# Optimization experiments

Measured on AMD Instinct MI355X. Metric: run time of the kernel, lower is better.

Reference implementation:

```python
import jax, jax.numpy as jnp
import numpy as np

E, S, H, D, B = 8, 64, 2048, 1024, 8192
LN_EPS = 1e-5


def setup_inputs() -> dict:
    key = jax.random.key(0)
    ks = jax.random.split(key, 12)
    n = lambda k, shape: jax.random.normal(k, shape, jnp.float32) * 0.02
    return {
        "raw_state": jax.random.normal(ks[0], (B, S), jnp.float32),
        "has_proprio": jax.random.randint(ks[1], (B,), 0, 2, jnp.int32),
        "expert_idx": jax.random.randint(ks[2], (B,), 0, E, jnp.int32),
        "pw1": n(ks[3], (E, S, H)), "pb1": jnp.zeros((E, H), jnp.float32),
        "pw2": n(ks[4], (E, H, D)), "pb2": jnp.zeros((E, D), jnp.float32),
        "qw1": n(ks[5], (E, S, H)), "qb1": jnp.zeros((E, H), jnp.float32),
        "qw2": n(ks[6], (E, H, D)), "qb2": jnp.zeros((E, D), jnp.float32),
        "ln_g": jnp.ones((E, D), jnp.float32), "ln_b": jnp.zeros((E, D), jnp.float32),
        "tw1": n(ks[7], (E, D, H)), "tb1": jnp.zeros((E, H), jnp.float32),
        "tw2": n(ks[8], (E, H, D)), "tb2": jnp.zeros((E, D), jnp.float32),
    }


def _gelu(x):
    # torch nn.GELU default = exact erf form
    return jax.nn.gelu(x, approximate=False)


def _expert_fwd(x, sel, w):
    (pw1, pb1, pw2, pb2, qw1, qb1, qw2, qb2, ln_g, ln_b, tw1, tb1, tw2, tb2) = w
    placeholder = _gelu(x @ pw1 + pb1) @ pw2 + pb2      # [B, D]
    proprio = _gelu(x @ qw1 + qb1) @ qw2 + qb2          # [B, D]
    mixed = placeholder * (1.0 - sel) + proprio * sel    # [B, D]
    mu = jnp.mean(mixed, axis=-1, keepdims=True)
    var = jnp.mean(jnp.square(mixed - mu), axis=-1, keepdims=True)
    normed = (mixed - mu) * jax.lax.rsqrt(var + LN_EPS) * ln_g + ln_b
    return _gelu(normed @ tw1 + tb1) @ tw2 + tb2         # [B, D]


def reference(raw_state, has_proprio, expert_idx,
              pw1, pb1, pw2, pb2, qw1, qb1, qw2, qb2,
              ln_g, ln_b, tw1, tb1, tw2, tb2):
    sel = has_proprio.astype(raw_state.dtype)[:, None]  # [B, 1]
    n_experts = pw1.shape[0]
    acc = jnp.zeros((raw_state.shape[0], tw2.shape[-1]), raw_state.dtype)
    # Fixed small loop over experts; rows routed via mask-select (same math
    # as the original index_select -> projector -> index_copy_).
    for e in range(n_experts):
        w = (pw1[e], pb1[e], pw2[e], pb2[e], qw1[e], qb1[e], qw2[e], qb2[e],
             ln_g[e], ln_b[e], tw1[e], tb1[e], tw2[e], tb2[e])
        oe = _expert_fwd(raw_state, sel, w)
        acc = jnp.where((expert_idx == e)[:, None], oe, acc)
    return acc[:, None, :]  # [B, 1, D]
```

## Files before the change

### kernel.cpp

```cpp
#include <hip/hip_runtime.h>
#include <math.h>

typedef unsigned short u16;
typedef unsigned int   u32;
typedef __attribute__((ext_vector_type(8))) short bh8;
typedef __attribute__((ext_vector_type(4))) float f4;

#define TM 128
#define TN 128
#define TK 32
#define LDT 40

__device__ __forceinline__ u16 f2b(float f) {
  u32 u = __builtin_bit_cast(u32, f);
  u += 0x7fffu + ((u >> 16) & 1u);
  return (u16)(u >> 16);
}
__device__ __forceinline__ float b2f(u16 b) {
  u32 u = ((u32)b) << 16;
  return __builtin_bit_cast(float, u);
}
__device__ __forceinline__ float gelu_f(float x) {
  return 0.5f * x * (1.0f + erff(x * 0.70710678118654752f));
}

__global__ __launch_bounds__(128) void init_routing(int* __restrict__ R) {
  R[threadIdx.x] = 0;
}

__global__ __launch_bounds__(256) void hist_kernel(const int* __restrict__ eidx,
                                                   const int* __restrict__ hasp,
                                                   int* __restrict__ R,
                                                   int* __restrict__ grp) {
  int t = blockIdx.x * 256 + threadIdx.x;
  int g = eidx[t] * 2 + (hasp[t] != 0 ? 1 : 0);
  grp[t] = g;
  atomicAdd(&R[g], 1);
}

__global__ __launch_bounds__(64) void scan_kernel(int* __restrict__ R) {
  if (threadIdx.x == 0) {
    int* cnt = R; int* cur = R + 16; int* gs = R + 32; int* to = R + 64;
    gs[0] = 0; to[0] = 0;
    for (int g = 0; g < 16; g++) {
      gs[g + 1] = gs[g] + cnt[g];
      cur[g] = gs[g];
      to[g + 1] = to[g] + (cnt[g] + TM - 1) / TM;
    }
  }
}

__global__ __launch_bounds__(256) void scatter_kernel(const int* __restrict__ grp,
                                                      int* __restrict__ R,
                                                      int* __restrict__ perm) {
  int t = blockIdx.x * 256 + threadIdx.x;
  int g = grp[t];
  int pos = atomicAdd(&R[16 + g], 1);
  perm[pos] = t;
}

__global__ __launch_bounds__(256) void gather_kernel(const float* __restrict__ raw,
                                                     const int* __restrict__ perm,
                                                     u16* __restrict__ Xg) {
  int t = blockIdx.x * 256 + threadIdx.x;
  int pos = t >> 6, ln = t & 63;
  int orig = perm[pos];
  Xg[(size_t)pos * 64 + ln] = f2b(raw[(size_t)orig * 64 + ln]);
}

__global__ __launch_bounds__(256) void transpose_cvt(const float* __restrict__ srcP,
                                                     const float* __restrict__ srcQ,
                                                     int twoSrc, int Rr, int Cc,
                                                     u16* __restrict__ dst) {
  int m = blockIdx.z;
  const float* src = twoSrc ? (((m & 1) ? srcQ : srcP) + (size_t)(m >> 1) * Rr * Cc)
                            : (srcP + (size_t)m * Rr * Cc);
  u16* d = dst + (size_t)m * Rr * Cc;
  __shared__ u16 t[32][34];
  int c0 = blockIdx.x * 32, r0 = blockIdx.y * 32;
  int tx = threadIdx.x, ty = threadIdx.y;
#pragma unroll
  for (int i = 0; i < 4; i++)
    t[ty + i * 8][tx] = f2b(src[(size_t)(r0 + ty + i * 8) * Cc + c0 + tx]);
  __syncthreads();
#pragma unroll
  for (int i = 0; i < 4; i++)
    d[(size_t)(c0 + ty + i * 8) * Rr + r0 + tx] = t[tx][ty + i * 8];
}

__global__ __launch_bounds__(256)
void gemm_grouped(const u16* __restrict__ A, int lda,
                  const u16* __restrict__ W, int wShift, int K, int N,
                  const float* __restrict__ biasP, const float* __restrict__ biasQ,
                  int branchBias, int doGelu,
                  u16* __restrict__ outB, float* __restrict__ outF,
                  int doScatter, int ldo,
                  const int* __restrict__ gstart, const int* __restrict__ tileOff,
                  const int* __restrict__ perm) {
  __shared__ u16 As[TM * LDT];
  __shared__ u16 Bs[TN * LDT];

  int bidM = blockIdx.x;
  int tot = tileOff[16];
  if (bidM >= tot) return;
  int g = 0;
  while (g < 15 && bidM >= tileOff[g + 1]) g++;
  int rowStart = gstart[g] + (bidM - tileOff[g]) * TM;
  int rowEnd = gstart[g + 1];

  const u16* Wg = W + (size_t)(g >> wShift) * N * K;
  int e = g >> 1;
  const float* bias = ((branchBias && (g & 1)) ? biasQ : biasP) + (size_t)e * N;

  int tid = threadIdx.x;
  int lane = tid & 63;
  int wv = tid >> 6;
  int wm = (wv >> 1) * 64, wn = (wv & 1) * 64;
  int l15 = lane & 15, l4 = lane >> 4;
  int colBase = blockIdx.y * TN;

  f4 acc[4][4];
#pragma unroll
  for (int i = 0; i < 4; i++)
#pragma unroll
    for (int j = 0; j < 4; j++) acc[i][j] = (f4){0.f, 0.f, 0.f, 0.f};

  int sRow = tid >> 2;
  int sKq = tid & 3;

  for (int k0 = 0; k0 < K; k0 += TK) {
    __syncthreads();
#pragma unroll
    for (int h = 0; h < 2; h++) {
      int r = sRow + h * 64;
      int gr = rowStart + r;
      int grc = gr < rowEnd ? gr : (rowEnd - 1);
      uint4 v = *reinterpret_cast<const uint4*>(A + (size_t)grc * lda + k0 + sKq * 8);
      *reinterpret_cast<uint4*>(&As[r * LDT + sKq * 8]) = v;
    }
#pragma unroll
    for (int h = 0; h < 2; h++) {
      int n = sRow + h * 64;
      uint4 v = *reinterpret_cast<const uint4*>(Wg + (size_t)(colBase + n) * K + k0 + sKq * 8);
      *reinterpret_cast<uint4*>(&Bs[n * LDT + sKq * 8]) = v;
    }
    __syncthreads();

    bh8 a[4], b[4];
#pragma unroll
    for (int i = 0; i < 4; i++)
      a[i] = *reinterpret_cast<const bh8*>(&As[(wm + i * 16 + l15) * LDT + l4 * 8]);
#pragma unroll
    for (int j = 0; j < 4; j++)
      b[j] = *reinterpret_cast<const bh8*>(&Bs[(wn + j * 16 + l15) * LDT + l4 * 8]);
#pragma unroll
    for (int i = 0; i < 4; i++)
#pragma unroll
      for (int j = 0; j < 4; j++)
        acc[i][j] = __builtin_amdgcn_mfma_f32_16x16x32_bf16(a[i], b[j], acc[i][j], 0, 0, 0);
  }

#pragma unroll
  for (int i = 0; i < 4; i++) {
#pragma unroll
    for (int r = 0; r < 4; r++) {
      int row = rowStart + wm + i * 16 + l4 * 4 + r;
      if (row < rowEnd) {
        int orow = doScatter ? perm[row] : row;
#pragma unroll
        for (int j = 0; j < 4; j++) {
          int col = colBase + wn + j * 16 + l15;
          float v = acc[i][j][r] + bias[col];
          if (doGelu) v = gelu_f(v);
          if (outF) outF[(size_t)orow * ldo + col] = v;
          else      outB[(size_t)orow * ldo + col] = f2b(v);
        }
      }
    }
  }
}

__global__ __launch_bounds__(256) void ln_kernel(const float* __restrict__ MIX,
                                                 u16* __restrict__ NRM,
                                                 const float* __restrict__ lng,
                                                 const float* __restrict__ lnb,
                                                 const int* __restrict__ gstart) {
  const int D = 1024;
  int pos = blockIdx.x;
  int g = 0;
  while (g < 15 && pos >= gstart[g + 1]) g++;
  int e = g >> 1;
  int tid = threadIdx.x;
  float x[4];
  float s = 0.f, s2 = 0.f;
#pragma unroll
  for (int i = 0; i < 4; i++) {
    float v = MIX[(size_t)pos * D + tid + i * 256];
    x[i] = v; s += v; s2 += v * v;
  }
#pragma unroll
  for (int off = 32; off >= 1; off >>= 1) {
    s += __shfl_down(s, off);
    s2 += __shfl_down(s2, off);
  }
  __shared__ float red[8];
  int wv = tid >> 6;
  if ((tid & 63) == 0) { red[wv] = s; red[4 + wv] = s2; }
  __syncthreads();
  if (tid == 0) {
    red[0] = red[0] + red[1] + red[2] + red[3];
    red[4] = red[4] + red[5] + red[6] + red[7];
  }
  __syncthreads();
  float mean = red[0] / D;
  float var = red[4] / D - mean * mean;
  float rstd = rsqrtf(var + 1e-5f);
#pragma unroll
  for (int i = 0; i < 4; i++) {
    int c = tid + i * 256;
    float v = (x[i] - mean) * rstd * lng[(size_t)e * D + c] + lnb[(size_t)e * D + c];
    NRM[(size_t)pos * D + c] = f2b(v);
  }
}

extern "C" void kernel_launch(void* const* d_in, const int* in_sizes, int n_in,
                              void* d_out, int out_size, void* d_ws, size_t ws_size,
                              hipStream_t stream) {
  const float* raw = (const float*)d_in[0];
  const int* hasp = (const int*)d_in[1];
  const int* eidx = (const int*)d_in[2];
  const float* pw1 = (const float*)d_in[3];  const float* pb1 = (const float*)d_in[4];
  const float* pw2 = (const float*)d_in[5];  const float* pb2 = (const float*)d_in[6];
  const float* qw1 = (const float*)d_in[7];  const float* qb1 = (const float*)d_in[8];
  const float* qw2 = (const float*)d_in[9];  const float* qb2 = (const float*)d_in[10];
  const float* lng = (const float*)d_in[11]; const float* lnb = (const float*)d_in[12];
  const float* tw1 = (const float*)d_in[13]; const float* tb1 = (const float*)d_in[14];
  const float* tw2 = (const float*)d_in[15]; const float* tb2 = (const float*)d_in[16];
  float* out = (float*)d_out;

  const int B = in_sizes[0] / 64;
  const int S = 64, H = 2048, D = 1024, E = 8;

  char* ws = (char*)d_ws;
  size_t o = 0;
  int* R    = (int*)(ws + o); o += 1024;
  int* grp  = (int*)(ws + o); o += (size_t)B * 4;
  int* perm = (int*)(ws + o); o += (size_t)B * 4;
  u16* Xg   = (u16*)(ws + o); o += (size_t)B * S * 2;
  u16* Hbuf = (u16*)(ws + o); o += (size_t)B * H * 2;
  float* MIX = (float*)(ws + o); o += (size_t)B * D * 4;
  u16* NRM  = (u16*)(ws + o); o += (size_t)B * D * 2;
  u16* W1T  = (u16*)(ws + o); o += (size_t)2 * E * S * H * 2;
  u16* WB   = (u16*)(ws + o);
  u16* T1T  = WB;
  u16* T2T  = WB + (size_t)E * D * H;

  int* gstart = R + 32;
  int* toff = R + 64;

  init_routing<<<1, 128, 0, stream>>>(R);
  hist_kernel<<<B / 256, 256, 0, stream>>>(eidx, hasp, R, grp);
  scan_kernel<<<1, 64, 0, stream>>>(R);
  scatter_kernel<<<B / 256, 256, 0, stream>>>(grp, R, perm);
  gather_kernel<<<B / 4, 256, 0, stream>>>(raw, perm, Xg);

  dim3 tb(32, 8);
  transpose_cvt<<<dim3(H / 32, S / 32, 16), tb, 0, stream>>>(pw1, qw1, 1, S, H, W1T);
  transpose_cvt<<<dim3(D / 32, H / 32, 16), tb, 0, stream>>>(pw2, qw2, 1, H, D, WB);

  const int maxT = B / TM + 16;
  gemm_grouped<<<dim3(maxT, H / TN), 256, 0, stream>>>(
      Xg, S, W1T, 0, S, H, pb1, qb1, 1, 1, Hbuf, nullptr, 0, H, gstart, toff, perm);
  gemm_grouped<<<dim3(maxT, D / TN), 256, 0, stream>>>(
      Hbuf, H, WB, 0, H, D, pb2, qb2, 1, 0, nullptr, MIX, 0, D, gstart, toff, perm);
  ln_kernel<<<B, 256, 0, stream>>>(MIX, NRM, lng, lnb, gstart);
  transpose_cvt<<<dim3(H / 32, D / 32, 8), tb, 0, stream>>>(tw1, nullptr, 0, D, H, T1T);
  transpose_cvt<<<dim3(D / 32, H / 32, 8), tb, 0, stream>>>(tw2, nullptr, 0, H, D, T2T);
  gemm_grouped<<<dim3(maxT, H / TN), 256, 0, stream>>>(
      NRM, D, T1T, 1, D, H, tb1, nullptr, 0, 1, Hbuf, nullptr, 0, H, gstart, toff, perm);
  gemm_grouped<<<dim3(maxT, D / TN), 256, 0, stream>>>(
      Hbuf, H, T2T, 1, H, D, tb2, nullptr, 0, 0, nullptr, out, 1, D, gstart, toff, perm);
}
```

Measured before the change: 674.0 us.

## Load GEMM tiles via direct global-to-LDS and enlarge transpose tiles

The grouped GEMM now stages A and B tiles with global_load_lds DMA instructions straight into unpadded shared memory, instead of loading into registers and storing to LDS. This removes the register round trip and the VGPR pressure of staging. The cost is that dropping the padding may cause LDS bank conflicts on the fragment reads. Separately, the weight transpose-and-convert kernel uses 64x64 tiles with a 64x4 thread block, so each block does more work and fewer blocks are launched.

```diff
diff --git a/kernel.cpp b/kernel.cpp
--- a/kernel.cpp
+++ b/kernel.cpp
@@ -9,19 +9,20 @@
 #define TM 128
 #define TN 128
 #define TK 32
-#define LDT 40
 
 __device__ __forceinline__ u16 f2b(float f) {
   u32 u = __builtin_bit_cast(u32, f);
   u += 0x7fffu + ((u >> 16) & 1u);
   return (u16)(u >> 16);
 }
-__device__ __forceinline__ float b2f(u16 b) {
-  u32 u = ((u32)b) << 16;
-  return __builtin_bit_cast(float, u);
-}
 __device__ __forceinline__ float gelu_f(float x) {
   return 0.5f * x * (1.0f + erff(x * 0.70710678118654752f));
+}
+
+__device__ __forceinline__ void gl2lds16(const u16* g, u16* l) {
+  __builtin_amdgcn_global_load_lds(
+      (const __attribute__((address_space(1))) u32*)g,
+      (__attribute__((address_space(3))) u32*)l, 16, 0, 0);
 }
 
 __global__ __launch_bounds__(128) void init_routing(int* __restrict__ R) {
@@ -76,16 +77,20 @@
   const float* src = twoSrc ? (((m & 1) ? srcQ : srcP) + (size_t)(m >> 1) * Rr * Cc)
                             : (srcP + (size_t)m * Rr * Cc);
   u16* d = dst + (size_t)m * Rr * Cc;
-  __shared__ u16 t[32][34];
-  int c0 = blockIdx.x * 32, r0 = blockIdx.y * 32;
+  __shared__ u16 t[64][66];
+  int c0 = blockIdx.x * 64, r0 = blockIdx.y * 64;
   int tx = threadIdx.x, ty = threadIdx.y;
 #pragma unroll
-  for (int i = 0; i < 4; i++)
-    t[ty + i * 8][tx] = f2b(src[(size_t)(r0 + ty + i * 8) * Cc + c0 + tx]);
+  for (int i = 0; i < 16; i++) {
+    int r = ty + i * 4;
+    t[tx][r] = f2b(src[(size_t)(r0 + r) * Cc + c0 + tx]);
+  }
   __syncthreads();
 #pragma unroll
-  for (int i = 0; i < 4; i++)
-    d[(size_t)(c0 + ty + i * 8) * Rr + r0 + tx] = t[tx][ty + i * 8];
+  for (int i = 0; i < 16; i++) {
+    int c = ty + i * 4;
+    d[(size_t)(c0 + c) * Rr + r0 + tx] = t[c][tx];
+  }
 }
 
 __global__ __launch_bounds__(256)
@@ -97,8 +102,8 @@
                   int doScatter, int ldo,
                   const int* __restrict__ gstart, const int* __restrict__ tileOff,
                   const int* __restrict__ perm) {
-  __shared__ u16 As[TM * LDT];
-  __shared__ u16 Bs[TN * LDT];
+  __shared__ __align__(16) u16 As[TM * TK];
+  __shared__ __align__(16) u16 Bs[TN * TK];
 
   int bidM = blockIdx.x;
   int tot = tileOff[16];
@@ -119,40 +124,42 @@
   int l15 = lane & 15, l4 = lane >> 4;
   int colBase = blockIdx.y * TN;
 
+  int cA = wv * 2;
+  int rA0 = cA * 16 + (lane >> 2);
+  int rA1 = rA0 + 16;
+  int kq8 = (lane & 3) * 8;
+  int grA0 = rowStart + rA0; grA0 = grA0 < rowEnd ? grA0 : (rowEnd - 1);
+  int grA1 = rowStart + rA1; grA1 = grA1 < rowEnd ? grA1 : (rowEnd - 1);
+  const u16* aSrc0 = A + (size_t)grA0 * lda + kq8;
+  const u16* aSrc1 = A + (size_t)grA1 * lda + kq8;
+  const u16* bSrc0 = Wg + (size_t)(colBase + rA0) * K + kq8;
+  const u16* bSrc1 = Wg + (size_t)(colBase + rA1) * K + kq8;
+  u16* aDst0 = &As[cA * 512];
+  u16* aDst1 = &As[cA * 512 + 512];
+  u16* bDst0 = &Bs[cA * 512];
+  u16* bDst1 = &Bs[cA * 512 + 512];
+
   f4 acc[4][4];
 #pragma unroll
   for (int i = 0; i < 4; i++)
 #pragma unroll
     for (int j = 0; j < 4; j++) acc[i][j] = (f4){0.f, 0.f, 0.f, 0.f};
-
-  int sRow = tid >> 2;
-  int sKq = tid & 3;
 
   for (int k0 = 0; k0 < K; k0 += TK) {
     __syncthreads();
-#pragma unroll
-    for (int h = 0; h < 2; h++) {
-      int r = sRow + h * 64;
-      int gr = rowStart + r;
-      int grc = gr < rowEnd ? gr : (rowEnd - 1);
-      uint4 v = *reinterpret_cast<const uint4*>(A + (size_t)grc * lda + k0 + sKq * 8);
-      *reinterpret_cast<uint4*>(&As[r * LDT + sKq * 8]) = v;
-    }
-#pragma unroll
-    for (int h = 0; h < 2; h++) {
-      int n = sRow + h * 64;
-      uint4 v = *reinterpret_cast<const uint4*>(Wg + (size_t)(colBase + n) * K + k0 + sKq * 8);
-      *reinterpret_cast<uint4*>(&Bs[n * LDT + sKq * 8]) = v;
-    }
+    gl2lds16(aSrc0 + k0, aDst0);
+    gl2lds16(aSrc1 + k0, aDst1);
+    gl2lds16(bSrc0 + k0, bDst0);
+    gl2lds16(bSrc1 + k0, bDst1);
     __syncthreads();
 
     bh8 a[4], b[4];
 #pragma unroll
     for (int i = 0; i < 4; i++)
-      a[i] = *reinterpret_cast<const bh8*>(&As[(wm + i * 16 + l15) * LDT + l4 * 8]);
+      a[i] = *reinterpret_cast<const bh8*>(&As[(wm + i * 16 + l15) * TK + l4 * 8]);
 #pragma unroll
     for (int j = 0; j < 4; j++)
-      b[j] = *reinterpret_cast<const bh8*>(&Bs[(wn + j * 16 + l15) * LDT + l4 * 8]);
+      b[j] = *reinterpret_cast<const bh8*>(&Bs[(wn + j * 16 + l15) * TK + l4 * 8]);
 #pragma unroll
     for (int i = 0; i < 4; i++)
 #pragma unroll
@@ -264,9 +271,9 @@
   scatter_kernel<<<B / 256, 256, 0, stream>>>(grp, R, perm);
   gather_kernel<<<B / 4, 256, 0, stream>>>(raw, perm, Xg);
 
-  dim3 tb(32, 8);
-  transpose_cvt<<<dim3(H / 32, S / 32, 16), tb, 0, stream>>>(pw1, qw1, 1, S, H, W1T);
-  transpose_cvt<<<dim3(D / 32, H / 32, 16), tb, 0, stream>>>(pw2, qw2, 1, H, D, WB);
+  dim3 tb(64, 4);
+  transpose_cvt<<<dim3(H / 64, S / 64, 16), tb, 0, stream>>>(pw1, qw1, 1, S, H, W1T);
+  transpose_cvt<<<dim3(D / 64, H / 64, 16), tb, 0, stream>>>(pw2, qw2, 1, H, D, WB);
 
   const int maxT = B / TM + 16;
   gemm_grouped<<<dim3(maxT, H / TN), 256, 0, stream>>>(
@@ -274,8 +281,8 @@
   gemm_grouped<<<dim3(maxT, D / TN), 256, 0, stream>>>(
       Hbuf, H, WB, 0, H, D, pb2, qb2, 1, 0, nullptr, MIX, 0, D, gstart, toff, perm);
   ln_kernel<<<B, 256, 0, stream>>>(MIX, NRM, lng, lnb, gstart);
-  transpose_cvt<<<dim3(H / 32, D / 32, 8), tb, 0, stream>>>(tw1, nullptr, 0, D, H, T1T);
-  transpose_cvt<<<dim3(D / 32, H / 32, 8), tb, 0, stream>>>(tw2, nullptr, 0, H, D, T2T);
+  transpose_cvt<<<dim3(H / 64, D / 64, 8), tb, 0, stream>>>(tw1, nullptr, 0, D, H, T1T);
+  transpose_cvt<<<dim3(D / 64, H / 64, 8), tb, 0, stream>>>(tw2, nullptr, 0, H, D, T2T);
   gemm_grouped<<<dim3(maxT, H / TN), 256, 0, stream>>>(
       NRM, D, T1T, 1, D, H, tb1, nullptr, 0, 1, Hbuf, nullptr, 0, H, gstart, toff, perm);
   gemm_grouped<<<dim3(maxT, D / TN), 256, 0, stream>>>(
```

Result: faster. 653.0 us (-3.1%).
